# Kernel tuning notes

Measured on AMD Instinct MI355X. Metric: run time of the kernel, lower is better.

## Reference

```python
import jax, jax.numpy as jnp
import numpy as np

B, L, D = 4, 2048, 1024
EV = 64            # event_embed_dim
EXPAND = 2
DI = EXPAND * D    # d_inner = 2048
N = 16             # d_state
K = 4              # d_conv
DT_RANK = (D + 15) // 16  # 64
EPS = 1e-5


def setup_inputs() -> dict:
    key = jax.random.key(0)
    ks = jax.random.split(key, 16)
    g = lambda k, shape, s=0.02: (jax.random.normal(k, shape, dtype=jnp.float32) * s)
    return {
        "x": jax.random.normal(ks[0], (B, L, D), dtype=jnp.float32),
        "event_emb": jax.random.normal(ks[1], (B, L, EV), dtype=jnp.float32),
        "W_in": g(ks[2], (D + EV, D)),
        "b_in": jnp.zeros((D,), jnp.float32),
        "ln_g": jnp.ones((D,), jnp.float32),
        "ln_b": jnp.zeros((D,), jnp.float32),
        "in_proj_w": g(ks[3], (D, 2 * DI)),
        "conv_w": g(ks[4], (DI, K), 0.1),
        "conv_b": jnp.zeros((DI,), jnp.float32),
        "x_proj_w": g(ks[5], (DI, DT_RANK + 2 * N)),
        "dt_proj_w": g(ks[6], (DT_RANK, DI), 0.1),
        "dt_proj_b": jnp.full((DI,), -4.6, jnp.float32),  # ~softplus^-1(0.01)
        "A_log": jnp.log(jnp.broadcast_to(jnp.arange(1, N + 1, dtype=jnp.float32), (DI, N))),
        "D_param": jnp.ones((DI,), jnp.float32),
        "out_proj_w": g(ks[7], (DI, D)),
    }


def _mamba_block(x, event_emb, W_in, b_in, ln_g, ln_b, in_proj_w, conv_w, conv_b,
                 x_proj_w, dt_proj_w, dt_proj_b, A_log, D_param, out_proj_w):
    d_conv = conv_w.shape[1]
    n_state = A_log.shape[1]
    dt_rank = dt_proj_w.shape[0]
    Lx = x.shape[1]

    aug = jnp.concatenate([x, event_emb], axis=-1) @ W_in + b_in   # [B,L,D]
    residual = aug
    mu = aug.mean(-1, keepdims=True)
    var = jnp.mean((aug - mu) ** 2, axis=-1, keepdims=True)
    h = (aug - mu) * jax.lax.rsqrt(var + EPS) * ln_g + ln_b

    xz = h @ in_proj_w                                             # [B,L,2*DI]
    xh, z = jnp.split(xz, 2, axis=-1)

    # causal depthwise conv1d (width d_conv)
    xp = jnp.pad(xh, ((0, 0), (d_conv - 1, 0), (0, 0)))
    xc = conv_b
    for k in range(d_conv):
        xc = xc + conv_w[:, k] * xp[:, k:k + Lx, :]
    xc = jax.nn.silu(xc)                                           # [B,L,DI]

    dbl = xc @ x_proj_w                                            # [B,L,dt_rank+2N]
    dt, Bm, Cm = jnp.split(dbl, [dt_rank, dt_rank + n_state], axis=-1)
    dt = jax.nn.softplus(dt @ dt_proj_w + dt_proj_b)               # [B,L,DI]
    A = -jnp.exp(A_log)                                            # [DI,N]

    def step(hst, inp):
        dt_t, B_t, C_t, u_t = inp                                  # [B,DI],[B,N],[B,N],[B,DI]
        dA = jnp.exp(dt_t[:, :, None] * A)                         # [B,DI,N]
        dBu = (dt_t * u_t)[:, :, None] * B_t[:, None, :]           # [B,DI,N]
        hst = dA * hst + dBu
        y_t = jnp.einsum('bdn,bn->bd', hst, C_t)
        return hst, y_t

    h0 = jnp.zeros((xc.shape[0], xc.shape[2], n_state), xc.dtype)
    xs = (dt.transpose(1, 0, 2), Bm.transpose(1, 0, 2),
          Cm.transpose(1, 0, 2), xc.transpose(1, 0, 2))
    _, ys = jax.lax.scan(step, h0, xs)                             # [L,B,DI]
    y = ys.transpose(1, 0, 2) + D_param * xc
    y = y * jax.nn.silu(z)
    return residual + y @ out_proj_w                               # [B,L,D]


def reference(x, event_emb, W_in, b_in, ln_g, ln_b, in_proj_w, conv_w, conv_b,
              x_proj_w, dt_proj_w, dt_proj_b, A_log, D_param, out_proj_w):
    return _mamba_block(x, event_emb, W_in, b_in, ln_g, ln_b, in_proj_w, conv_w,
                        conv_b, x_proj_w, dt_proj_w, dt_proj_b, A_log, D_param,
                        out_proj_w)
```

## Files before the change

### kernel.cpp

```cpp
#include <hip/hip_runtime.h>
#include <cstdint>
#include <cstddef>

#define DEV __device__ __forceinline__

typedef __bf16 bf16x8 __attribute__((ext_vector_type(8)));
typedef float f32x4 __attribute__((ext_vector_type(4)));

DEV unsigned short f2bf(float f) {
  unsigned u = __builtin_bit_cast(unsigned, f);
  u += 0x7fffu + ((u >> 16) & 1u);
  return (unsigned short)(u >> 16);
}
DEV float bf2f(unsigned short h) {
  return __builtin_bit_cast(float, (unsigned)h << 16);
}

__global__ __launch_bounds__(256)
void k_concat(const float* __restrict__ x, const float* __restrict__ ev,
              unsigned short* __restrict__ Aaug) {
  int col4 = blockIdx.x * 256 + threadIdx.x;
  if (col4 >= 288) return;
  size_t row = blockIdx.y;
  float4 v = make_float4(0.f, 0.f, 0.f, 0.f);
  if (col4 < 256)      v = reinterpret_cast<const float4*>(x + row * 1024)[col4];
  else if (col4 < 272) v = reinterpret_cast<const float4*>(ev + row * 64)[col4 - 256];
  ushort4 o; o.x = f2bf(v.x); o.y = f2bf(v.y); o.z = f2bf(v.z); o.w = f2bf(v.w);
  reinterpret_cast<ushort4*>(Aaug + row * 1152)[col4] = o;
}

__global__ void k_transpose(const float* __restrict__ in, unsigned short* __restrict__ out,
                            int R, int C, int Rout, int Cout) {
  __shared__ float tile[32][33];
  int c0 = blockIdx.x * 32, r0 = blockIdx.y * 32;
  int tx = threadIdx.x, ty = threadIdx.y;
#pragma unroll
  for (int i = 0; i < 4; ++i) {
    int r = r0 + ty + i * 8, c = c0 + tx;
    tile[ty + i * 8][tx] = (r < R && c < C) ? in[(size_t)r * C + c] : 0.f;
  }
  __syncthreads();
#pragma unroll
  for (int i = 0; i < 4; ++i) {
    int c = c0 + ty + i * 8, r = r0 + tx;
    if (c < Cout && r < Rout) out[(size_t)c * Rout + r] = f2bf(tile[tx][ty + i * 8]);
  }
}

template <int BN, int EPI>
__global__ __launch_bounds__(512, 1)
void k_gemm8(const unsigned short* __restrict__ A, const unsigned short* __restrict__ Bt,
             int N, int NT, int lda, int ldb,
             float* __restrict__ outF, unsigned short* __restrict__ outB1,
             unsigned short* __restrict__ outB2,
             const float* __restrict__ bias, const float* __restrict__ resid) {
  static_assert(BN == 128 || BN == 256, "");
  constexpr int NF = BN / 64;
  constexpr int NHF = NF / 2;
  constexpr int BLOADS = BN / 128;
  constexpr int ATILE = 256 * 64;
  constexpr int BTILE = BN * 64;
  constexpr int BUFSZ = ATILE + BTILE;
  __shared__ unsigned short lds[2 * BUFSZ];

  const int tid = threadIdx.x;
  const int lane = tid & 63, w = tid >> 6;
  const int wm = w >> 2, wn = w & 3;
  const int frow = lane & 15, fk = lane >> 4;

  const int nbx = gridDim.x;
  const int nwg = nbx * gridDim.y;
  const int orig = blockIdx.y * nbx + blockIdx.x;
  const int swz = (orig & 7) * (nwg >> 3) + (orig >> 3);
  const int brow = swz / nbx, bcol = swz % nbx;
  const size_t row0 = (size_t)brow * 256, col0 = (size_t)bcol * BN;

  f32x4 acc[8][NF];
#pragma unroll
  for (int i = 0; i < 8; ++i)
#pragma unroll
    for (int j = 0; j < NF; ++j) acc[i][j] = f32x4{0.f, 0.f, 0.f, 0.f};

  bf16x8 afr[4][2], bq0[NHF][2], bq1[NHF][2];

  const int srow = tid >> 3;
  const int g8 = ((tid & 7) ^ (srow & 7)) * 8;
  const size_t offA_h0l0 = (row0 + 0 * 128 + 0 * 64 + srow) * (size_t)lda + g8;
  const size_t offA_h0l1 = (row0 + 1 * 128 + 0 * 64 + srow) * (size_t)lda + g8;
  const size_t offA_h1l0 = (row0 + 0 * 128 + 1 * 64 + srow) * (size_t)lda + g8;
  const size_t offA_h1l1 = (row0 + 1 * 128 + 1 * 64 + srow) * (size_t)lda + g8;
  const size_t offB_h0l0 = (col0 + 0 * (BN / 2) + 0 * 64 + srow) * (size_t)ldb + g8;
  const size_t offB_h1l0 = (col0 + 1 * (BN / 2) + 0 * 64 + srow) * (size_t)ldb + g8;
  const size_t offB_h0l1 = (BLOADS == 2) ? ((col0 + 0 * (BN / 2) + 1 * 64 + srow) * (size_t)ldb + g8) : 0;
  const size_t offB_h1l1 = (BLOADS == 2) ? ((col0 + 1 * (BN / 2) + 1 * 64 + srow) * (size_t)ldb + g8) : 0;

  char* ldsb = reinterpret_cast<char*>(lds);
  const int fr7 = frow & 7;
  const int slot0 = (fk ^ fr7) * 16;
  const int slot1 = ((4 + fk) ^ fr7) * 16;
  const int abase0 = (wm * 128 + frow) * 128 + slot0;
  const int abase1 = (wm * 128 + frow) * 128 + slot1;
  const int bbase0 = (wn * (BN / 4) + frow) * 128 + slot0 + ATILE * 2;
  const int bbase1 = (wn * (BN / 4) + frow) * 128 + slot1 + ATILE * 2;

  auto stageA = [&](int p, int tau, int half) {
    const size_t kadd = (size_t)tau * 64;
    const unsigned short* s0 = A + (half ? offA_h1l0 : offA_h0l0) + kadd;
    const unsigned short* s1 = A + (half ? offA_h1l1 : offA_h0l1) + kadd;
    unsigned short* dst = lds + p * BUFSZ + half * 4096 + w * 512;
    __builtin_amdgcn_global_load_lds(s0, dst, 16, 0, 0);
    __builtin_amdgcn_global_load_lds(s1, dst + 8192, 16, 0, 0);
  };
  auto stageB = [&](int p, int tau, int half) {
    const size_t kadd = (size_t)tau * 64;
    unsigned short* dst = lds + p * BUFSZ + ATILE + half * (BTILE / 2) + w * 512;
    const unsigned short* s0 = Bt + (half ? offB_h1l0 : offB_h0l0) + kadd;
    __builtin_amdgcn_global_load_lds(s0, dst, 16, 0, 0);
    if constexpr (BLOADS == 2) {
      const unsigned short* s1 = Bt + (half ? offB_h1l1 : offB_h0l1) + kadd;
      __builtin_amdgcn_global_load_lds(s1, dst + 4096, 16, 0, 0);
    }
  };
  auto ldA = [&](int p, int mh) {
    const int pb = p * (BUFSZ * 2);
#pragma unroll
    for (int mi = 0; mi < 4; ++mi) {
      const int off = pb + (mh * 64 + mi * 16) * 128;
      afr[mi][0] = *reinterpret_cast<const bf16x8*>(ldsb + abase0 + off);
      afr[mi][1] = *reinterpret_cast<const bf16x8*>(ldsb + abase1 + off);
    }
  };
  auto ldB = [&](int p, int nh, bf16x8 (&bq)[NHF][2]) {
    const int pb = p * (BUFSZ * 2);
#pragma unroll
    for (int ni = 0; ni < NHF; ++ni) {
      const int off = pb + (nh * (BN / 8) + ni * 16) * 128;
      bq[ni][0] = *reinterpret_cast<const bf16x8*>(ldsb + bbase0 + off);
      bq[ni][1] = *reinterpret_cast<const bf16x8*>(ldsb + bbase1 + off);
    }
  };

#define MMAQ(MH, NH, BQ)                                                          \
  do {                                                                            \
    _Pragma("unroll") for (int mi = 0; mi < 4; ++mi)                              \
        _Pragma("unroll") for (int ni = 0; ni < NHF; ++ni)                        \
            _Pragma("unroll") for (int kb = 0; kb < 2; ++kb)                      \
                acc[(MH)*4 + mi][(NH)*NHF + ni] =                                 \
                    __builtin_amdgcn_mfma_f32_16x16x32_bf16(                      \
                        afr[mi][kb], BQ[ni][kb], acc[(MH)*4 + mi][(NH)*NHF + ni], \
                        0, 0, 0);                                                 \
  } while (0)

#define PRIO1 __builtin_amdgcn_s_setprio(1)
#define PRIO0 __builtin_amdgcn_s_setprio(0)
#define BARC  __builtin_amdgcn_s_barrier()
#define SBAR  __builtin_amdgcn_sched_barrier(0)
#define VMCNT_WAIT                                                     \
  do {                                                                 \
    if constexpr (BN == 256)                                           \
      asm volatile("s_waitcnt vmcnt(6)" ::: "memory");                 \
    else                                                               \
      asm volatile("s_waitcnt vmcnt(4)" ::: "memory");                 \
  } while (0)

  stageA(0, 0, 0); stageB(0, 0, 0); stageB(0, 0, 1); stageA(0, 0, 1);
  SBAR;
  stageA(1, 1, 0); stageB(1, 1, 0); stageB(1, 1, 1);
  VMCNT_WAIT;
  BARC; SBAR;

  const int niter = NT >> 1;
  for (int it = 0; it < niter; ++it) {
    int t = 2 * it;
    int t1s = t + 1;
    int t2s = (t + 2 < NT) ? t + 2 : NT - 1;
    int t3s = (t + 3 < NT) ? t + 3 : NT - 1;
    ldA(0, 0); ldB(0, 0, bq0); ldB(0, 1, bq1);
    stageA(1, t1s, 1);
    BARC; PRIO1; MMAQ(0, 0, bq0); MMAQ(0, 1, bq1); PRIO0; BARC;
    ldA(0, 1);
    stageA(0, t2s, 0); stageB(0, t2s, 0); stageB(0, t2s, 1);
    VMCNT_WAIT;
    BARC; PRIO1; MMAQ(1, 1, bq1); MMAQ(1, 0, bq0); PRIO0; BARC;
    ldA(1, 0); ldB(1, 0, bq0); ldB(1, 1, bq1);
    stageA(0, t2s, 1);
    BARC; PRIO1; MMAQ(0, 0, bq0); MMAQ(0, 1, bq1); PRIO0; BARC;
    ldA(1, 1);
    stageA(1, t3s, 0); stageB(1, t3s, 0); stageB(1, t3s, 1);
    VMCNT_WAIT;
    BARC; PRIO1; MMAQ(1, 1, bq1); MMAQ(1, 0, bq0); PRIO0; BARC;
  }

#pragma unroll
  for (int q = 0; q < 8; ++q) {
#pragma unroll
    for (int j = 0; j < NF; ++j) {
#pragma unroll
      for (int r = 0; r < 4; ++r) {
        size_t row = row0 + wm * 128 + q * 16 + fk * 4 + r;
        size_t col = col0 + wn * (BN / 4) + j * 16 + frow;
        float v = acc[q][j][r];
        if constexpr (EPI == 0) {
          outF[row * N + col] = v + bias[col];
        } else if constexpr (EPI == 1) {
          int hn = N >> 1;
          if ((int)col < hn) outB1[row * hn + col] = f2bf(v);
          else               outB2[row * hn + (col - hn)] = f2bf(v);
        } else {
          outF[row * N + col] = resid[row * N + col] + v;
        }
      }
    }
  }
#undef MMAQ
#undef PRIO1
#undef PRIO0
#undef BARC
#undef SBAR
#undef VMCNT_WAIT
}

template <int EPI>
__global__ __launch_bounds__(256)
void k_gemm(const unsigned short* __restrict__ A, const unsigned short* __restrict__ Bt,
            int N, int K, int lda, int ldb,
            unsigned short* __restrict__ outB1, const float* __restrict__ bias) {
  __shared__ alignas(16) unsigned short sA[128 * 64];
  __shared__ alignas(16) unsigned short sB[128 * 64];
  int tid = threadIdx.x;
  int lane = tid & 63, w = tid >> 6;
  int nbx = gridDim.x;
  int nwg = nbx * gridDim.y;
  int orig = blockIdx.y * nbx + blockIdx.x;
  int swz = (orig & 7) * (nwg >> 3) + (orig >> 3);
  int brow = swz / nbx, bcol = swz % nbx;
  size_t row0 = (size_t)brow * 128, col0 = (size_t)bcol * 128;

  int lrow_s = tid >> 3;
  int g_s = tid & 7;
  int wrow = (w >> 1) * 64, wcol = (w & 1) * 64;
  int frow = lane & 15, fk = lane >> 4;
  f32x4 acc[4][4] = {};

  for (int kt = 0; kt < K; kt += 64) {
    __syncthreads();
#pragma unroll
    for (int r = 0; r < 4; ++r) {
      int lr = r * 32 + lrow_s;
      int gs = g_s ^ (lr & 7);
      const unsigned short* srcA = A + (size_t)(row0 + lr) * lda + kt + gs * 8;
      const unsigned short* srcB = Bt + (size_t)(col0 + lr) * ldb + kt + gs * 8;
      unsigned short* dstA = sA + (r * 32 + w * 8) * 64;
      unsigned short* dstB = sB + (r * 32 + w * 8) * 64;
      __builtin_amdgcn_global_load_lds(srcA, dstA, 16, 0, 0);
      __builtin_amdgcn_global_load_lds(srcB, dstB, 16, 0, 0);
    }
    __syncthreads();
#pragma unroll
    for (int kw = 0; kw < 2; ++kw) {
      bf16x8 af[4], bfr[4];
      int gk = kw * 4 + fk;
#pragma unroll
      for (int mi = 0; mi < 4; ++mi) {
        int rr = wrow + mi * 16 + frow;
        af[mi] = *reinterpret_cast<const bf16x8*>(sA + rr * 64 + ((gk ^ (rr & 7)) * 8));
      }
#pragma unroll
      for (int ni = 0; ni < 4; ++ni) {
        int rr = wcol + ni * 16 + frow;
        bfr[ni] = *reinterpret_cast<const bf16x8*>(sB + rr * 64 + ((gk ^ (rr & 7)) * 8));
      }
#pragma unroll
      for (int mi = 0; mi < 4; ++mi)
#pragma unroll
        for (int ni = 0; ni < 4; ++ni)
          acc[mi][ni] = __builtin_amdgcn_mfma_f32_16x16x32_bf16(af[mi], bfr[ni], acc[mi][ni], 0, 0, 0);
    }
  }

#pragma unroll
  for (int mi = 0; mi < 4; ++mi) {
#pragma unroll
    for (int ni = 0; ni < 4; ++ni) {
#pragma unroll
      for (int r = 0; r < 4; ++r) {
        size_t row = row0 + wrow + mi * 16 + fk * 4 + r;
        size_t col = col0 + wcol + ni * 16 + frow;
        float v = acc[mi][ni][r];
        if constexpr (EPI == 2) {
          outB1[row * N + col] = f2bf(v);
        } else {
          float xx = v + bias[col];
          float sp = (xx > 15.f) ? xx : __logf(1.f + __expf(xx));
          outB1[row * N + col] = f2bf(sp);
        }
      }
    }
  }
}

__global__ __launch_bounds__(256)
void k_ln(const float* __restrict__ aug, const float* __restrict__ gam,
          const float* __restrict__ bet, unsigned short* __restrict__ h) {
  int tid = threadIdx.x;
  size_t row = blockIdx.x;
  float4 v = reinterpret_cast<const float4*>(aug + row * 1024)[tid];
  float s = v.x + v.y + v.z + v.w;
  float ss = v.x * v.x + v.y * v.y + v.z * v.z + v.w * v.w;
#pragma unroll
  for (int m = 32; m >= 1; m >>= 1) {
    s += __shfl_xor(s, m, 64);
    ss += __shfl_xor(ss, m, 64);
  }
  __shared__ float rb[8];
  if ((tid & 63) == 0) { rb[tid >> 6] = s; rb[4 + (tid >> 6)] = ss; }
  __syncthreads();
  float ts = rb[0] + rb[1] + rb[2] + rb[3];
  float tss = rb[4] + rb[5] + rb[6] + rb[7];
  float mu = ts * (1.f / 1024.f);
  float var = tss * (1.f / 1024.f) - mu * mu;
  float rs = rsqrtf(var + 1e-5f);
  float4 gv = reinterpret_cast<const float4*>(gam)[tid];
  float4 bv = reinterpret_cast<const float4*>(bet)[tid];
  ushort4 o;
  o.x = f2bf((v.x - mu) * rs * gv.x + bv.x);
  o.y = f2bf((v.y - mu) * rs * gv.y + bv.y);
  o.z = f2bf((v.z - mu) * rs * gv.z + bv.z);
  o.w = f2bf((v.w - mu) * rs * gv.w + bv.w);
  reinterpret_cast<ushort4*>(h + row * 1024)[tid] = o;
}

__global__ __launch_bounds__(256)
void k_conv(const unsigned short* __restrict__ xh, const float* __restrict__ cw,
            const float* __restrict__ cb, unsigned short* __restrict__ xc) {
  size_t row = blockIdx.x;
  int t = (int)(row & 2047);
  size_t rowb = row - t;
  int d = threadIdx.x * 8;
  float acc[8];
  {
    float4 c0 = *reinterpret_cast<const float4*>(cb + d);
    float4 c1 = *reinterpret_cast<const float4*>(cb + d + 4);
    acc[0] = c0.x; acc[1] = c0.y; acc[2] = c0.z; acc[3] = c0.w;
    acc[4] = c1.x; acc[5] = c1.y; acc[6] = c1.z; acc[7] = c1.w;
  }
  float wv[8][4];
#pragma unroll
  for (int j = 0; j < 8; ++j) {
    float4 cj = *reinterpret_cast<const float4*>(cw + (size_t)(d + j) * 4);
    wv[j][0] = cj.x; wv[j][1] = cj.y; wv[j][2] = cj.z; wv[j][3] = cj.w;
  }
#pragma unroll
  for (int k = 0; k < 4; ++k) {
    int tt = t - 3 + k;
    if (tt >= 0) {
      ushort4 va = reinterpret_cast<const ushort4*>(xh + (rowb + tt) * 2048 + d)[0];
      ushort4 vb = reinterpret_cast<const ushort4*>(xh + (rowb + tt) * 2048 + d)[1];
      unsigned short e[8] = {va.x, va.y, va.z, va.w, vb.x, vb.y, vb.z, vb.w};
#pragma unroll
      for (int j = 0; j < 8; ++j) acc[j] += wv[j][k] * bf2f(e[j]);
    }
  }
  ushort4 o0, o1;
#pragma unroll
  for (int j = 0; j < 8; ++j) {
    float sg = 1.f / (1.f + __expf(-acc[j]));
    unsigned short r = f2bf(acc[j] * sg);
    if (j < 4) (&o0.x)[j] = r; else (&o1.x)[j - 4] = r;
  }
  reinterpret_cast<ushort4*>(xc + row * 2048 + d)[0] = o0;
  reinterpret_cast<ushort4*>(xc + row * 2048 + d)[1] = o1;
}

template <bool FINAL>
__global__ __launch_bounds__(256)
void k_scan(const unsigned short* __restrict__ dt, const unsigned short* __restrict__ xc,
            const unsigned short* __restrict__ dbl, const float* __restrict__ A_log,
            float* __restrict__ S, float* __restrict__ SD,
            const float* __restrict__ Hin, const float* __restrict__ Dp,
            const unsigned short* __restrict__ z, unsigned short* __restrict__ yg) {
  int d = blockIdx.x * 256 + threadIdx.x;
  int b = blockIdx.y, c = blockIdx.z;
  int t0 = c * 32;
  size_t hoff = (((size_t)c * 4 + b) * 2048 + d) * 16;
  float An[16], h[16];
  bool fast = true;
#pragma unroll
  for (int n = 0; n < 16; ++n) {
    An[n] = -__expf(A_log[((size_t)d << 4) + n]);
    fast = fast && (__builtin_fabsf(An[n] + (float)(n + 1)) < 1e-4f);
    h[n] = FINAL ? Hin[hoff + n] : 0.f;
  }
  float Dv = FINAL ? Dp[d] : 0.f;
  float dts = 0.f;
  __shared__ float sBC[32][32];
  if (threadIdx.x < 128) {
    int s = threadIdx.x >> 2, j8 = (threadIdx.x & 3) * 8;
    size_t rowg = (size_t)b * 2048 + t0 + s;
    uint4 raw = *reinterpret_cast<const uint4*>(dbl + rowg * 128 + 64 + j8);
    unsigned rr4[4] = {raw.x, raw.y, raw.z, raw.w};
#pragma unroll
    for (int q = 0; q < 4; ++q) {
      sBC[s][j8 + 2 * q]     = bf2f((unsigned short)(rr4[q] & 0xffffu));
      sBC[s][j8 + 2 * q + 1] = bf2f((unsigned short)(rr4[q] >> 16));
    }
  }
  __syncthreads();

  if (fast) {
    for (int si = 0; si < 32; ++si) {
      size_t rr = ((size_t)b * 2048 + t0 + si) * 2048 + d;
      float dtv = bf2f(dt[rr]);
      float uv = bf2f(xc[rr]);
      float dtu = dtv * uv;
      float y = 0.f;
      if constexpr (!FINAL) dts += dtv;
      float e1 = __expf(-dtv);
      float e2 = e1 * e1;
      float e3 = e2 * e1, e4 = e2 * e2;
      float e8 = e4 * e4, e12 = e8 * e4;
      float base[4] = {e1, e2, e3, e4};
      float mul[4] = {1.f, e4, e8, e12};
#pragma unroll
      for (int n = 0; n < 16; ++n) {
        float a = base[n & 3] * mul[n >> 2];
        h[n] = a * h[n] + dtu * sBC[si][n];
        if constexpr (FINAL) y += h[n] * sBC[si][16 + n];
      }
      if constexpr (FINAL) {
        float zv = bf2f(z[rr]);
        float sig = 1.f / (1.f + __expf(-zv));
        yg[rr] = f2bf((y + Dv * uv) * (zv * sig));
      }
    }
  } else {
    for (int si = 0; si < 32; ++si) {
      size_t rr = ((size_t)b * 2048 + t0 + si) * 2048 + d;
      float dtv = bf2f(dt[rr]);
      float uv = bf2f(xc[rr]);
      float dtu = dtv * uv;
      float y = 0.f;
      if constexpr (!FINAL) dts += dtv;
#pragma unroll
      for (int n = 0; n < 16; ++n) {
        float a = __expf(dtv * An[n]);
        h[n] = a * h[n] + dtu * sBC[si][n];
        if constexpr (FINAL) y += h[n] * sBC[si][16 + n];
      }
      if constexpr (FINAL) {
        float zv = bf2f(z[rr]);
        float sig = 1.f / (1.f + __expf(-zv));
        yg[rr] = f2bf((y + Dv * uv) * (zv * sig));
      }
    }
  }
  if constexpr (!FINAL) {
#pragma unroll
    for (int n = 0; n < 16; ++n) S[hoff + n] = h[n];
    SD[((size_t)c * 4 + b) * 2048 + d] = dts;
  }
}

__global__ __launch_bounds__(256)
void k_scanB(float* __restrict__ S, const float* __restrict__ SD,
             const float* __restrict__ A_log) {
  int id = blockIdx.x * 256 + threadIdx.x;
  int n = id & 15, d = (id >> 4) & 2047, b = id >> 15;
  float An = -__expf(A_log[((size_t)d << 4) + n]);
  float h = 0.f;
  for (int c = 0; c < 64; ++c) {
    size_t sdo = ((size_t)c * 4 + b) * 2048 + d;
    size_t o = sdo * 16 + n;
    float s = S[o];
    float p = __expf(An * SD[sdo]);
    S[o] = h;
    h = s + p * h;
  }
}

extern "C" void kernel_launch(void* const* d_in, const int* in_sizes, int n_in,
                              void* d_out, int out_size, void* d_ws, size_t ws_size,
                              hipStream_t stream) {
  const float* x       = (const float*)d_in[0];
  const float* ev      = (const float*)d_in[1];
  const float* W_in    = (const float*)d_in[2];
  const float* b_in    = (const float*)d_in[3];
  const float* ln_g    = (const float*)d_in[4];
  const float* ln_b    = (const float*)d_in[5];
  const float* in_proj = (const float*)d_in[6];
  const float* conv_w  = (const float*)d_in[7];
  const float* conv_b  = (const float*)d_in[8];
  const float* x_proj  = (const float*)d_in[9];
  const float* dt_proj = (const float*)d_in[10];
  const float* dt_b    = (const float*)d_in[11];
  const float* A_log   = (const float*)d_in[12];
  const float* D_par   = (const float*)d_in[13];
  const float* out_w   = (const float*)d_in[14];
  float* out = (float*)d_out;

  char* ws = (char*)d_ws;
  size_t off = 0;
  auto alloc = [&](size_t bytes) {
    char* p = ws + off;
    off = (off + bytes + 255) & ~(size_t)255;
    return p;
  };
  float* aug            = (float*)alloc(8192ull * 1024 * 4);
  unsigned short* dtfb  = (unsigned short*)alloc(8192ull * 2048 * 2);
  unsigned short* Aaug  = (unsigned short*)alloc(8192ull * 1152 * 2);
  unsigned short* WinT  = (unsigned short*)alloc(1024ull * 1152 * 2);
  unsigned short* ipT   = (unsigned short*)alloc(4096ull * 1024 * 2);
  unsigned short* xpT   = (unsigned short*)alloc(128ull * 2048 * 2);
  unsigned short* dpT   = (unsigned short*)alloc(2048ull * 64 * 2);
  unsigned short* opT   = (unsigned short*)alloc(1024ull * 2048 * 2);
  unsigned short* xh    = (unsigned short*)alloc(8192ull * 2048 * 2);
  unsigned short* zb    = (unsigned short*)alloc(8192ull * 2048 * 2);
  unsigned short* xcb   = (unsigned short*)alloc(8192ull * 2048 * 2);
  unsigned short* dbl   = (unsigned short*)alloc(8192ull * 128 * 2);
  float* Sb = (float*)alloc(64ull * 4 * 2048 * 16 * 4);
  float* SD = (float*)alloc(64ull * 4 * 2048 * 4);
  unsigned short* hb = Aaug;
  unsigned short* yg = xh;

  k_concat<<<dim3(2, 8192), 256, 0, stream>>>(x, ev, Aaug);
  k_transpose<<<dim3(32, 36), dim3(32, 8), 0, stream>>>(W_in, WinT, 1088, 1024, 1152, 1024);
  k_transpose<<<dim3(128, 32), dim3(32, 8), 0, stream>>>(in_proj, ipT, 1024, 4096, 1024, 4096);
  k_transpose<<<dim3(4, 64), dim3(32, 8), 0, stream>>>(x_proj, xpT, 2048, 96, 2048, 128);
  k_transpose<<<dim3(64, 2), dim3(32, 8), 0, stream>>>(dt_proj, dpT, 64, 2048, 64, 2048);
  k_transpose<<<dim3(32, 64), dim3(32, 8), 0, stream>>>(out_w, opT, 2048, 1024, 2048, 1024);

  k_gemm8<128, 0><<<dim3(8, 32), 512, 0, stream>>>(Aaug, WinT, 1024, 18, 1152, 1152,
                                                   aug, nullptr, nullptr, b_in, nullptr);
  k_ln<<<dim3(8192), 256, 0, stream>>>(aug, ln_g, ln_b, hb);
  k_gemm8<256, 1><<<dim3(16, 32), 512, 0, stream>>>(hb, ipT, 4096, 16, 1024, 1024,
                                                    nullptr, xh, zb, nullptr, nullptr);
  k_conv<<<dim3(8192), 256, 0, stream>>>(xh, conv_w, conv_b, xcb);
  k_gemm<2><<<dim3(1, 64), 256, 0, stream>>>(xcb, xpT, 128, 2048, 2048, 2048, dbl, nullptr);
  k_gemm<3><<<dim3(16, 64), 256, 0, stream>>>(dbl, dpT, 2048, 64, 128, 64, dtfb, dt_b);
  k_scan<false><<<dim3(8, 4, 64), 256, 0, stream>>>(dtfb, xcb, dbl, A_log, Sb, SD,
                                                    nullptr, nullptr, nullptr, nullptr);
  k_scanB<<<dim3(512), 256, 0, stream>>>(Sb, SD, A_log);
  k_scan<true><<<dim3(8, 4, 64), 256, 0, stream>>>(dtfb, xcb, dbl, A_log, nullptr, nullptr,
                                                   Sb, D_par, zb, yg);
  k_gemm8<128, 4><<<dim3(8, 32), 512, 0, stream>>>(yg, opT, 1024, 32, 2048, 2048,
                                                   out, nullptr, nullptr, nullptr, aug);
}
```

Measured before the change: 404.3 us.

## Merge prep kernels, store aug in bf16, split-K the x_proj GEMM

Replaces the concat kernel and five weight-transpose launches with a single k_prep launch that dispatches on block index. The first GEMM now writes the residual/aug tensor as bf16, which halves its write and its two later reads (LayerNorm and the final residual add) at the cost of residual precision. The x_proj GEMM, which had only 64 blocks, is split two ways along K into fp32 partials and reduced by a new k_comb kernel. This adds parallelism at the price of an extra launch and extra traffic.

```diff
diff --git a/kernel.cpp b/kernel.cpp
--- a/kernel.cpp
+++ b/kernel.cpp
@@ -16,24 +16,40 @@
   return __builtin_bit_cast(float, (unsigned)h << 16);
 }
 
-__global__ __launch_bounds__(256)
-void k_concat(const float* __restrict__ x, const float* __restrict__ ev,
-              unsigned short* __restrict__ Aaug) {
-  int col4 = blockIdx.x * 256 + threadIdx.x;
-  if (col4 >= 288) return;
-  size_t row = blockIdx.y;
-  float4 v = make_float4(0.f, 0.f, 0.f, 0.f);
-  if (col4 < 256)      v = reinterpret_cast<const float4*>(x + row * 1024)[col4];
-  else if (col4 < 272) v = reinterpret_cast<const float4*>(ev + row * 64)[col4 - 256];
-  ushort4 o; o.x = f2bf(v.x); o.y = f2bf(v.y); o.z = f2bf(v.z); o.w = f2bf(v.w);
-  reinterpret_cast<ushort4*>(Aaug + row * 1152)[col4] = o;
-}
-
-__global__ void k_transpose(const float* __restrict__ in, unsigned short* __restrict__ out,
-                            int R, int C, int Rout, int Cout) {
+struct TransJob { const float* in; unsigned short* out; int R, C, Rout, Cout, gx; };
+
+__global__ __launch_bounds__(256)
+void k_prep(const float* __restrict__ x, const float* __restrict__ ev,
+            unsigned short* __restrict__ Aaug,
+            const float* __restrict__ W_in, unsigned short* __restrict__ WinT,
+            const float* __restrict__ ipW, unsigned short* __restrict__ ipT,
+            const float* __restrict__ xpW, unsigned short* __restrict__ xpT,
+            const float* __restrict__ dpW, unsigned short* __restrict__ dpT,
+            const float* __restrict__ opW, unsigned short* __restrict__ opT) {
+  int tid = threadIdx.x;
+  int idx = blockIdx.x;
+  if (idx < 16384) {
+    int col4 = (idx & 1) * 256 + tid;
+    if (col4 >= 288) return;
+    size_t row = idx >> 1;
+    float4 v = make_float4(0.f, 0.f, 0.f, 0.f);
+    if (col4 < 256)      v = reinterpret_cast<const float4*>(x + row * 1024)[col4];
+    else if (col4 < 272) v = reinterpret_cast<const float4*>(ev + row * 64)[col4 - 256];
+    ushort4 o; o.x = f2bf(v.x); o.y = f2bf(v.y); o.z = f2bf(v.z); o.w = f2bf(v.w);
+    reinterpret_cast<ushort4*>(Aaug + row * 1152)[col4] = o;
+    return;
+  }
+  idx -= 16384;
+  const float* in; unsigned short* out; int R, C, Rout, Cout, gx;
+  if (idx < 1152)      { in = W_in; out = WinT; R = 1088; C = 1024; Rout = 1152; Cout = 1024; gx = 32; }
+  else if ((idx -= 1152) < 4096) { in = ipW; out = ipT; R = 1024; C = 4096; Rout = 1024; Cout = 4096; gx = 128; }
+  else if ((idx -= 4096) < 256)  { in = xpW; out = xpT; R = 2048; C = 96;   Rout = 2048; Cout = 128;  gx = 4;   }
+  else if ((idx -= 256) < 128)   { in = dpW; out = dpT; R = 64;   C = 2048; Rout = 64;   Cout = 2048; gx = 64;  }
+  else                 { idx -= 128; in = opW; out = opT; R = 2048; C = 1024; Rout = 2048; Cout = 1024; gx = 32; }
+  int cx = idx % gx, ry = idx / gx;
   __shared__ float tile[32][33];
-  int c0 = blockIdx.x * 32, r0 = blockIdx.y * 32;
-  int tx = threadIdx.x, ty = threadIdx.y;
+  int c0 = cx * 32, r0 = ry * 32;
+  int tx = tid & 31, ty = tid >> 5;
 #pragma unroll
   for (int i = 0; i < 4; ++i) {
     int r = r0 + ty + i * 8, c = c0 + tx;
@@ -53,7 +69,7 @@
              int N, int NT, int lda, int ldb,
              float* __restrict__ outF, unsigned short* __restrict__ outB1,
              unsigned short* __restrict__ outB2,
-             const float* __restrict__ bias, const float* __restrict__ resid) {
+             const float* __restrict__ bias, const unsigned short* __restrict__ residB) {
   static_assert(BN == 128 || BN == 256, "");
   constexpr int NF = BN / 64;
   constexpr int NHF = NF / 2;
@@ -201,13 +217,13 @@
         size_t col = col0 + wn * (BN / 4) + j * 16 + frow;
         float v = acc[q][j][r];
         if constexpr (EPI == 0) {
-          outF[row * N + col] = v + bias[col];
+          outB1[row * N + col] = f2bf(v + bias[col]);
         } else if constexpr (EPI == 1) {
           int hn = N >> 1;
           if ((int)col < hn) outB1[row * hn + col] = f2bf(v);
           else               outB2[row * hn + (col - hn)] = f2bf(v);
         } else {
-          outF[row * N + col] = resid[row * N + col] + v;
+          outF[row * N + col] = bf2f(residB[row * N + col]) + v;
         }
       }
     }
@@ -224,7 +240,8 @@
 __global__ __launch_bounds__(256)
 void k_gemm(const unsigned short* __restrict__ A, const unsigned short* __restrict__ Bt,
             int N, int K, int lda, int ldb,
-            unsigned short* __restrict__ outB1, const float* __restrict__ bias) {
+            unsigned short* __restrict__ outB1, const float* __restrict__ bias,
+            float* __restrict__ outF) {
   __shared__ alignas(16) unsigned short sA[128 * 64];
   __shared__ alignas(16) unsigned short sB[128 * 64];
   int tid = threadIdx.x;
@@ -235,6 +252,9 @@
   int swz = (orig & 7) * (nwg >> 3) + (orig >> 3);
   int brow = swz / nbx, bcol = swz % nbx;
   size_t row0 = (size_t)brow * 128, col0 = (size_t)bcol * 128;
+  int ks = 0;
+  if constexpr (EPI == 6) { ks = bcol; col0 = 0; }
+  const size_t kbase = (size_t)ks * 1024;
 
   int lrow_s = tid >> 3;
   int g_s = tid & 7;
@@ -248,8 +268,8 @@
     for (int r = 0; r < 4; ++r) {
       int lr = r * 32 + lrow_s;
       int gs = g_s ^ (lr & 7);
-      const unsigned short* srcA = A + (size_t)(row0 + lr) * lda + kt + gs * 8;
-      const unsigned short* srcB = Bt + (size_t)(col0 + lr) * ldb + kt + gs * 8;
+      const unsigned short* srcA = A + (size_t)(row0 + lr) * lda + kbase + kt + gs * 8;
+      const unsigned short* srcB = Bt + (size_t)(col0 + lr) * ldb + kbase + kt + gs * 8;
       unsigned short* dstA = sA + (r * 32 + w * 8) * 64;
       unsigned short* dstB = sB + (r * 32 + w * 8) * 64;
       __builtin_amdgcn_global_load_lds(srcA, dstA, 16, 0, 0);
@@ -287,8 +307,8 @@
         size_t row = row0 + wrow + mi * 16 + fk * 4 + r;
         size_t col = col0 + wcol + ni * 16 + frow;
         float v = acc[mi][ni][r];
-        if constexpr (EPI == 2) {
-          outB1[row * N + col] = f2bf(v);
+        if constexpr (EPI == 6) {
+          outF[(size_t)ks * (8192ull * 128) + row * 128 + col] = v;
         } else {
           float xx = v + bias[col];
           float sp = (xx > 15.f) ? xx : __logf(1.f + __expf(xx));
@@ -300,13 +320,25 @@
 }
 
 __global__ __launch_bounds__(256)
-void k_ln(const float* __restrict__ aug, const float* __restrict__ gam,
+void k_comb(const float* __restrict__ P, unsigned short* __restrict__ dbl) {
+  size_t i4 = (size_t)blockIdx.x * 256 + threadIdx.x;
+  float4 a = reinterpret_cast<const float4*>(P)[i4];
+  float4 b = reinterpret_cast<const float4*>(P + 8192ull * 128)[i4];
+  ushort4 o;
+  o.x = f2bf(a.x + b.x); o.y = f2bf(a.y + b.y);
+  o.z = f2bf(a.z + b.z); o.w = f2bf(a.w + b.w);
+  reinterpret_cast<ushort4*>(dbl)[i4] = o;
+}
+
+__global__ __launch_bounds__(256)
+void k_ln(const unsigned short* __restrict__ aug, const float* __restrict__ gam,
           const float* __restrict__ bet, unsigned short* __restrict__ h) {
   int tid = threadIdx.x;
   size_t row = blockIdx.x;
-  float4 v = reinterpret_cast<const float4*>(aug + row * 1024)[tid];
-  float s = v.x + v.y + v.z + v.w;
-  float ss = v.x * v.x + v.y * v.y + v.z * v.z + v.w * v.w;
+  ushort4 raw = reinterpret_cast<const ushort4*>(aug + row * 1024)[tid];
+  float v0 = bf2f(raw.x), v1 = bf2f(raw.y), v2 = bf2f(raw.z), v3 = bf2f(raw.w);
+  float s = v0 + v1 + v2 + v3;
+  float ss = v0 * v0 + v1 * v1 + v2 * v2 + v3 * v3;
 #pragma unroll
   for (int m = 32; m >= 1; m >>= 1) {
     s += __shfl_xor(s, m, 64);
@@ -323,10 +355,10 @@
   float4 gv = reinterpret_cast<const float4*>(gam)[tid];
   float4 bv = reinterpret_cast<const float4*>(bet)[tid];
   ushort4 o;
-  o.x = f2bf((v.x - mu) * rs * gv.x + bv.x);
-  o.y = f2bf((v.y - mu) * rs * gv.y + bv.y);
-  o.z = f2bf((v.z - mu) * rs * gv.z + bv.z);
-  o.w = f2bf((v.w - mu) * rs * gv.w + bv.w);
+  o.x = f2bf((v0 - mu) * rs * gv.x + bv.x);
+  o.y = f2bf((v1 - mu) * rs * gv.y + bv.y);
+  o.z = f2bf((v2 - mu) * rs * gv.z + bv.z);
+  o.w = f2bf((v3 - mu) * rs * gv.w + bv.w);
   reinterpret_cast<ushort4*>(h + row * 1024)[tid] = o;
 }
 
@@ -505,7 +537,7 @@
     off = (off + bytes + 255) & ~(size_t)255;
     return p;
   };
-  float* aug            = (float*)alloc(8192ull * 1024 * 4);
+  unsigned short* augb  = (unsigned short*)alloc(8192ull * 1024 * 2);
   unsigned short* dtfb  = (unsigned short*)alloc(8192ull * 2048 * 2);
   unsigned short* Aaug  = (unsigned short*)alloc(8192ull * 1152 * 2);
   unsigned short* WinT  = (unsigned short*)alloc(1024ull * 1152 * 2);
@@ -517,31 +549,31 @@
   unsigned short* zb    = (unsigned short*)alloc(8192ull * 2048 * 2);
   unsigned short* xcb   = (unsigned short*)alloc(8192ull * 2048 * 2);
   unsigned short* dbl   = (unsigned short*)alloc(8192ull * 128 * 2);
+  float* Pd = (float*)alloc(2ull * 8192 * 128 * 4);
   float* Sb = (float*)alloc(64ull * 4 * 2048 * 16 * 4);
   float* SD = (float*)alloc(64ull * 4 * 2048 * 4);
   unsigned short* hb = Aaug;
   unsigned short* yg = xh;
 
-  k_concat<<<dim3(2, 8192), 256, 0, stream>>>(x, ev, Aaug);
-  k_transpose<<<dim3(32, 36), dim3(32, 8), 0, stream>>>(W_in, WinT, 1088, 1024, 1152, 1024);
-  k_transpose<<<dim3(128, 32), dim3(32, 8), 0, stream>>>(in_proj, ipT, 1024, 4096, 1024, 4096);
-  k_transpose<<<dim3(4, 64), dim3(32, 8), 0, stream>>>(x_proj, xpT, 2048, 96, 2048, 128);
-  k_transpose<<<dim3(64, 2), dim3(32, 8), 0, stream>>>(dt_proj, dpT, 64, 2048, 64, 2048);
-  k_transpose<<<dim3(32, 64), dim3(32, 8), 0, stream>>>(out_w, opT, 2048, 1024, 2048, 1024);
+  k_prep<<<dim3(24064), 256, 0, stream>>>(x, ev, Aaug, W_in, WinT, in_proj, ipT,
+                                          x_proj, xpT, dt_proj, dpT, out_w, opT);
 
   k_gemm8<128, 0><<<dim3(8, 32), 512, 0, stream>>>(Aaug, WinT, 1024, 18, 1152, 1152,
-                                                   aug, nullptr, nullptr, b_in, nullptr);
-  k_ln<<<dim3(8192), 256, 0, stream>>>(aug, ln_g, ln_b, hb);
+                                                   nullptr, augb, nullptr, b_in, nullptr);
+  k_ln<<<dim3(8192), 256, 0, stream>>>(augb, ln_g, ln_b, hb);
   k_gemm8<256, 1><<<dim3(16, 32), 512, 0, stream>>>(hb, ipT, 4096, 16, 1024, 1024,
                                                     nullptr, xh, zb, nullptr, nullptr);
   k_conv<<<dim3(8192), 256, 0, stream>>>(xh, conv_w, conv_b, xcb);
-  k_gemm<2><<<dim3(1, 64), 256, 0, stream>>>(xcb, xpT, 128, 2048, 2048, 2048, dbl, nullptr);
-  k_gemm<3><<<dim3(16, 64), 256, 0, stream>>>(dbl, dpT, 2048, 64, 128, 64, dtfb, dt_b);
+  k_gemm<6><<<dim3(2, 64), 256, 0, stream>>>(xcb, xpT, 128, 1024, 2048, 2048,
+                                             nullptr, nullptr, Pd);
+  k_comb<<<dim3(1024), 256, 0, stream>>>(Pd, dbl);
+  k_gemm<3><<<dim3(16, 64), 256, 0, stream>>>(dbl, dpT, 2048, 64, 128, 64,
+                                              dtfb, dt_b, nullptr);
   k_scan<false><<<dim3(8, 4, 64), 256, 0, stream>>>(dtfb, xcb, dbl, A_log, Sb, SD,
                                                     nullptr, nullptr, nullptr, nullptr);
   k_scanB<<<dim3(512), 256, 0, stream>>>(Sb, SD, A_log);
   k_scan<true><<<dim3(8, 4, 64), 256, 0, stream>>>(dtfb, xcb, dbl, A_log, nullptr, nullptr,
                                                    Sb, D_par, zb, yg);
   k_gemm8<128, 4><<<dim3(8, 32), 512, 0, stream>>>(yg, opT, 1024, 32, 2048, 2048,
-                                                   out, nullptr, nullptr, nullptr, aug);
-}
+                                                   out, nullptr, nullptr, nullptr, augb);
+}
```

New measurement: 378.4 us. -6.4%, faster.
